# Optimization experiments

Hardware: AMD Instinct MI355X
Metric: run time of the kernel (lower is better)

Reference implementation:

```python
import jax, jax.numpy as jnp
import numpy as np

N_NODES = 100000
N_EDGES = 3200000
IN_DIM = 128
OUT_DIM = 128
BN_EPS = 1e-5
FILL_VALUE = 1.0  # improved_gcn=False -> self-loop weight 1.0 (2.0 if improved)


def setup_inputs() -> dict:
    key = jax.random.key(0)
    k1, k2, k3, k4 = jax.random.split(key, 4)
    node_features = jax.random.normal(k1, (N_NODES, IN_DIM), dtype=jnp.float32)
    edge_index = jax.random.randint(k2, (2, N_EDGES), 0, N_NODES, dtype=jnp.int64)
    edge_weight = jax.random.uniform(k3, (N_EDGES,), dtype=jnp.float32)
    # Glorot init like PyG GCNConv
    W = jax.random.normal(k4, (IN_DIM, OUT_DIM), dtype=jnp.float32) * np.sqrt(2.0 / (IN_DIM + OUT_DIM))
    b = jnp.zeros((OUT_DIM,), dtype=jnp.float32)
    gamma = jnp.ones((OUT_DIM,), dtype=jnp.float32)
    beta = jnp.zeros((OUT_DIM,), dtype=jnp.float32)
    return {"node_features": node_features, "edge_index": edge_index,
            "edge_weight": edge_weight, "W": W, "b": b, "gamma": gamma, "beta": beta}


def reference(node_features, edge_index, edge_weight, W, b, gamma, beta):
    N = node_features.shape[0]
    dt = node_features.dtype
    # --- gcn_norm: add self loops, symmetric normalization ---
    loop = jnp.arange(N, dtype=edge_index.dtype)
    row = jnp.concatenate([edge_index[0], loop])  # source
    col = jnp.concatenate([edge_index[1], loop])  # target (aggregation dim)
    w = jnp.concatenate([edge_weight.astype(dt), jnp.full((N,), FILL_VALUE, dtype=dt)])
    deg = jax.ops.segment_sum(w, col, num_segments=N)
    dinv = jnp.where(deg > 0, jax.lax.rsqrt(deg), 0.0).astype(dt)
    norm = dinv[row] * w * dinv[col]  # [E+N]
    # --- linear transform then message passing (scatter-add into targets) ---
    x = node_features @ W  # [N, out_dim]
    msg = x[row] * norm[:, None]  # [E+N, out_dim] gather
    out = jax.ops.segment_sum(msg, col, num_segments=N) + b
    # --- relu ---
    h = jax.nn.relu(out)
    # --- BatchNorm1d (training-mode batch statistics, biased variance) ---
    mean = jnp.mean(h, axis=0)
    var = jnp.mean(jnp.square(h - mean), axis=0)
    h = (h - mean) * jax.lax.rsqrt(var + BN_EPS) * gamma + beta
    # dropout is identity in eval / deterministic reference
    return h
```

## Files before the change

### kernel.cpp

```cpp
#include <hip/hip_runtime.h>
#include <hip/hip_bf16.h>


#define BKT_BITS 7
#define BKT_SZ 128
#define MAX_BKT 1024
#define CHUNK 8192

typedef __attribute__((ext_vector_type(8))) short bf16x8;
typedef __attribute__((ext_vector_type(4))) float f32x4;

__device__ __forceinline__ unsigned bf16rn(float f) {
    unsigned x = __float_as_uint(f);
    return (x + 0x7fffu + ((x >> 16) & 1u)) >> 16;
}
__device__ __forceinline__ float bflo(unsigned u) { return __uint_as_float(u << 16); }
__device__ __forceinline__ float bfhi(unsigned u) { return __uint_as_float(u & 0xffff0000u); }

__global__ __launch_bounds__(256) void k_bhist2(const int* __restrict__ col,
        int* __restrict__ blkoff, const float* __restrict__ Wm,
        unsigned* __restrict__ WT, int E, int nb, int nbc) {
    __shared__ int h[MAX_BKT];
    for (int i = threadIdx.x; i < nb; i += 256) h[i] = 0;
    __syncthreads();
    int base = blockIdx.x * CHUNK, lim = min(base + CHUNK, E);
    for (int e = base + threadIdx.x; e < lim; e += 256)
        atomicAdd(&h[col[e] >> BKT_BITS], 1);
    __syncthreads();
    for (int i = threadIdx.x; i < nb; i += 256)
        blkoff[(size_t)i * nbc + blockIdx.x] = h[i];
    if (blockIdx.x == 0) {
        for (int i = threadIdx.x; i < 128 * 64; i += 256) {
            int j = i >> 6, w = i & 63;
            float a = Wm[(size_t)(2 * w) * 128 + j];
            float b = Wm[(size_t)(2 * w + 1) * 128 + j];
            WT[i] = bf16rn(a) | (bf16rn(b) << 16);
        }
    }
}

__global__ void k_bscan2a(int* __restrict__ blkoff, int* __restrict__ btot,
                          int nb, int nbc) {
    int b = blockIdx.x * 256 + threadIdx.x;
    if (b >= nb) return;
    int* p = blkoff + (size_t)b * nbc;
    int run = 0;
#pragma unroll 4
    for (int i = 0; i < nbc; ++i) { int c = p[i]; p[i] = run; run += c; }
    btot[b] = run;
}

__global__ __launch_bounds__(1024) void k_bscan2b(const int* __restrict__ btot,
        int* __restrict__ bbase, int* __restrict__ ptr, float* __restrict__ sums,
        int nb, int N, int E) {
    __shared__ int ls[1024];
    int t = threadIdx.x;
    int v = (t < nb) ? btot[t] : 0;
    ls[t] = v;
    __syncthreads();
    for (int off = 1; off < 1024; off <<= 1) {
        int u = (t >= off) ? ls[t - off] : 0;
        __syncthreads();
        ls[t] += u;
        __syncthreads();
    }
    if (t < nb) bbase[t] = ls[t] - v;
    if (t == nb - 1) bbase[nb] = ls[t];
    if (t == 0) ptr[N] = E;
    if (t < 512) sums[t] = 0.0f;
}

__global__ __launch_bounds__(256) void k_passA3(
        const int* __restrict__ row, const int* __restrict__ col,
        const float* __restrict__ w, const int* __restrict__ blkoff,
        const int* __restrict__ bbase, unsigned* __restrict__ tmp,
        int E, int nb, int nbc) {
    __shared__ int cur[MAX_BKT];
    for (int i = threadIdx.x; i < nb; i += 256)
        cur[i] = bbase[i] + blkoff[(size_t)i * nbc + blockIdx.x];
    __syncthreads();
    int base = blockIdx.x * CHUNK, lim = min(base + CHUNK, E);
    for (int e = base + threadIdx.x; e < lim; e += 256) {
        int c = col[e];
        int q8 = (int)(w[e] * 256.0f + 0.5f);
        if (q8 > 255) q8 = 255;
        unsigned rec = ((unsigned)row[e] << 15) | ((unsigned)(c & 127) << 8) | (unsigned)q8;
        int pos = atomicAdd(&cur[c >> BKT_BITS], 1);
        tmp[pos] = rec;
    }
}

__global__ __launch_bounds__(256) void k_passB2(
        const unsigned* __restrict__ tmp, const int* __restrict__ bbase,
        unsigned* __restrict__ packed, int* __restrict__ ptr,
        float* __restrict__ dinv, int N) {
    __shared__ int hcnt[BKT_SZ];
    __shared__ int wsumi[BKT_SZ];
    __shared__ int cur[BKT_SZ];
    __shared__ float dcl[BKT_SZ];
    int b = blockIdx.x;
    int t = threadIdx.x;
    if (t < BKT_SZ) { hcnt[t] = 0; wsumi[t] = 0; }
    __syncthreads();
    int beg = bbase[b], end = bbase[b + 1];
    for (int k = beg + t; k < end; k += 256) {
        unsigned p = tmp[k];
        int li = (p >> 8) & 127;
        atomicAdd(&hcnt[li], 1);
        atomicAdd(&wsumi[li], (int)(p & 255u));
    }
    __syncthreads();
    if (t < BKT_SZ) cur[t] = hcnt[t];
    __syncthreads();
    for (int off = 1; off < BKT_SZ; off <<= 1) {
        int v = (t < BKT_SZ && t >= off) ? cur[t - off] : 0;
        __syncthreads();
        if (t < BKT_SZ) cur[t] += v;
        __syncthreads();
    }
    if (t < BKT_SZ) {
        int p = beg + cur[t] - hcnt[t];
        cur[t] = p;
        float d = 1.0f + (float)wsumi[t] * (1.0f / 256.0f);
        float dc = rsqrtf(d);
        dcl[t] = dc;
        int n = (b << BKT_BITS) + t;
        if (n < N) { ptr[n] = p; dinv[n] = dc; }
    }
    __syncthreads();
    for (int k = beg + t; k < end; k += 256) {
        unsigned p = tmp[k];
        int li = (p >> 8) & 127;
        int pos = atomicAdd(&cur[li], 1);
        float fw = (float)(p & 255u) * (1.0f / 256.0f) * dcl[li];
        unsigned wb = bf16rn(fw) & 0x7FFFu;
        packed[pos] = ((p >> 15) << 15) | wb;
    }
}

__global__ void k_conv2(const float* __restrict__ nf, const float* __restrict__ dinv,
                        uint4* __restrict__ tab, int N) {
    size_t i = (size_t)blockIdx.x * 256 + threadIdx.x;
    if (i >= (size_t)N * 16) return;
    int n = (int)(i >> 4);
    float dv = dinv[n];
    const float4* src = (const float4*)nf + 2 * i;
    float4 a = src[0], b = src[1];
    uint4 r;
    r.x = bf16rn(a.x * dv) | (bf16rn(a.y * dv) << 16);
    r.y = bf16rn(a.z * dv) | (bf16rn(a.w * dv) << 16);
    r.z = bf16rn(b.x * dv) | (bf16rn(b.y * dv) << 16);
    r.w = bf16rn(b.z * dv) | (bf16rn(b.w * dv) << 16);
    tab[i] = r;
}

#define EDGE_FMA(aX, nX, tX)                                     \
    aX[0] += nX * bflo(tX.x); aX[1] += nX * bfhi(tX.x);          \
    aX[2] += nX * bflo(tX.y); aX[3] += nX * bfhi(tX.y);          \
    aX[4] += nX * bflo(tX.z); aX[5] += nX * bfhi(tX.z);          \
    aX[6] += nX * bflo(tX.w); aX[7] += nX * bfhi(tX.w);

__global__ __launch_bounds__(256) void k_gatherq(
        const unsigned* __restrict__ packed, const int* __restrict__ ptr,
        const float* __restrict__ dinv, const unsigned* __restrict__ tab,
        unsigned* __restrict__ aggb, int N) {
    int lane = threadIdx.x & 63;
    int q = lane >> 4, fl = lane & 15;
    int wid = (int)(((size_t)blockIdx.x * 256 + threadIdx.x) >> 6);
    int node = wid * 4 + q;
    if (node >= N) return;
    int beg = ptr[node], end = ptr[node + 1];
    float dc = dinv[node];
    float a0[8] = {}, a1[8] = {}, a2[8] = {}, a3[8] = {};
    int k = beg;
    for (; k + 4 <= end; k += 4) {
        unsigned p0 = packed[k];
        unsigned p1 = packed[k + 1];
        unsigned p2 = packed[k + 2];
        unsigned p3 = packed[k + 3];
        uint4 t0 = *(const uint4*)(tab + (size_t)(p0 >> 15) * 64 + fl * 4);
        uint4 t1 = *(const uint4*)(tab + (size_t)(p1 >> 15) * 64 + fl * 4);
        uint4 t2 = *(const uint4*)(tab + (size_t)(p2 >> 15) * 64 + fl * 4);
        uint4 t3 = *(const uint4*)(tab + (size_t)(p3 >> 15) * 64 + fl * 4);
        float n0 = bflo(p0 & 0x7FFFu);
        float n1 = bflo(p1 & 0x7FFFu);
        float n2 = bflo(p2 & 0x7FFFu);
        float n3 = bflo(p3 & 0x7FFFu);
        EDGE_FMA(a0, n0, t0)
        EDGE_FMA(a1, n1, t1)
        EDGE_FMA(a2, n2, t2)
        EDGE_FMA(a3, n3, t3)
    }
    for (; k < end; ++k) {
        unsigned p = packed[k];
        uint4 t = *(const uint4*)(tab + (size_t)(p >> 15) * 64 + fl * 4);
        float n = bflo(p & 0x7FFFu);
        EDGE_FMA(a0, n, t)
    }
    {
        uint4 t = *(const uint4*)(tab + (size_t)node * 64 + fl * 4);
        EDGE_FMA(a0, dc, t)
    }
#pragma unroll
    for (int j = 0; j < 8; ++j) a0[j] = (a0[j] + a1[j]) + (a2[j] + a3[j]);
    uint4 r;
    r.x = bf16rn(a0[0]) | (bf16rn(a0[1]) << 16);
    r.y = bf16rn(a0[2]) | (bf16rn(a0[3]) << 16);
    r.z = bf16rn(a0[4]) | (bf16rn(a0[5]) << 16);
    r.w = bf16rn(a0[6]) | (bf16rn(a0[7]) << 16);
    *(uint4*)(aggb + (size_t)node * 64 + fl * 4) = r;
}

__global__ __launch_bounds__(256) void k_gatherwF(
        const unsigned* __restrict__ packed, const int* __restrict__ ptr,
        const float* __restrict__ dinv, const unsigned* __restrict__ tab,
        float* __restrict__ out, int N) {
    int wid = (int)(((size_t)blockIdx.x * 256 + threadIdx.x) >> 6);
    int lane = threadIdx.x & 63;
    if (wid >= N) return;
    int beg = ptr[wid], end = ptr[wid + 1];
    float dc = dinv[wid];
    int q = lane >> 4;
    int fl = lane & 15;
    float a0[8] = {}, a1[8] = {};
    int k = beg;
    for (; k + 8 <= end; k += 8) {
        unsigned p0 = packed[k + q];
        unsigned p1 = packed[k + 4 + q];
        uint4 t0 = *(const uint4*)(tab + (size_t)(p0 >> 15) * 64 + fl * 4);
        uint4 t1 = *(const uint4*)(tab + (size_t)(p1 >> 15) * 64 + fl * 4);
        float n0 = bflo(p0 & 0x7FFFu);
        float n1 = bflo(p1 & 0x7FFFu);
        EDGE_FMA(a0, n0, t0)
        EDGE_FMA(a1, n1, t1)
    }
    for (; k < end; k += 4) {
        int i0 = k + q;
        if (i0 < end) {
            unsigned p0 = packed[i0];
            uint4 t0 = *(const uint4*)(tab + (size_t)(p0 >> 15) * 64 + fl * 4);
            float n0 = bflo(p0 & 0x7FFFu);
            EDGE_FMA(a0, n0, t0)
        }
    }
#pragma unroll
    for (int j = 0; j < 8; ++j) {
        float s = a0[j] + a1[j];
        s += __shfl_xor(s, 16);
        s += __shfl_xor(s, 32);
        a0[j] = s;
    }
    if (q == 0) {
        uint4 t = *(const uint4*)(tab + (size_t)wid * 64 + fl * 4);
        EDGE_FMA(a0, dc, t)
        float4* dst = (float4*)(out + (size_t)wid * 128 + fl * 8);
        dst[0] = make_float4(a0[0], a0[1], a0[2], a0[3]);
        dst[1] = make_float4(a0[4], a0[5], a0[6], a0[7]);
    }
}

__global__ __launch_bounds__(256) void k_gemm3b(
        unsigned* aggb, const unsigned* __restrict__ WT,
        const float* __restrict__ bias, float* __restrict__ sums, int N) {
    __shared__ unsigned A_l[128][68];
    __shared__ unsigned W_l[128][68];
    __shared__ float bs[256];
    int tid = threadIdx.x;
    int r0 = blockIdx.x * 128;
    bs[tid] = 0.0f;
    {
        int j = tid >> 1, h = tid & 1;
        const uint4* src = (const uint4*)(WT + j * 64 + h * 32);
#pragma unroll
        for (int i = 0; i < 8; ++i)
            *(uint4*)&W_l[j][h * 32 + i * 4] = src[i];
    }
    {
        int j = tid >> 1, h = tid & 1;
        int gr = r0 + j;
        if (gr < N) {
            const uint4* src = (const uint4*)(aggb + (size_t)gr * 64 + h * 32);
#pragma unroll
            for (int i = 0; i < 8; ++i)
                *(uint4*)&A_l[j][h * 32 + i * 4] = src[i];
        } else {
            uint4 z = {0, 0, 0, 0};
#pragma unroll
            for (int i = 0; i < 8; ++i)
                *(uint4*)&A_l[j][h * 32 + i * 4] = z;
        }
    }
    __syncthreads();

    int wv = tid >> 6, l = tid & 63;
    int lr = l & 15, lk = l >> 4;
    f32x4 acc[2][8] = {};
#pragma unroll
    for (int ks = 0; ks < 4; ++ks) {
        bf16x8 a0 = *(bf16x8*)&A_l[wv * 32 + lr][ks * 16 + lk * 4];
        bf16x8 a1 = *(bf16x8*)&A_l[wv * 32 + 16 + lr][ks * 16 + lk * 4];
#pragma unroll
        for (int nt = 0; nt < 8; ++nt) {
            bf16x8 b = *(bf16x8*)&W_l[nt * 16 + lr][ks * 16 + lk * 4];
            acc[0][nt] = __builtin_amdgcn_mfma_f32_16x16x32_bf16(a0, b, acc[0][nt], 0, 0, 0);
            acc[1][nt] = __builtin_amdgcn_mfma_f32_16x16x32_bf16(a1, b, acc[1][nt], 0, 0, 0);
        }
    }

    unsigned short* ab = (unsigned short*)aggb;
#pragma unroll
    for (int nt = 0; nt < 8; ++nt) {
        int colc = nt * 16 + lr;
        float bc = bias[colc];
        float s = 0.0f, sq = 0.0f;
#pragma unroll
        for (int ms = 0; ms < 2; ++ms) {
#pragma unroll
            for (int p = 0; p < 4; ++p) {
                int rrow = r0 + wv * 32 + ms * 16 + lk * 4 + p;
                float v = fmaxf(acc[ms][nt][p] + bc, 0.0f);
                if (rrow < N) {
                    ab[(size_t)rrow * 128 + colc] = (unsigned short)bf16rn(v);
                    s += v;
                    sq += v * v;
                }
            }
        }
        s += __shfl_xor(s, 16);  s += __shfl_xor(s, 32);
        sq += __shfl_xor(sq, 16); sq += __shfl_xor(sq, 32);
        if (l < 16) {
            atomicAdd(&bs[colc], s);
            atomicAdd(&bs[128 + colc], sq);
        }
    }
    __syncthreads();
    if (tid < 128) {
        atomicAdd(&sums[tid], bs[tid]);
        atomicAdd(&sums[128 + tid], bs[128 + tid]);
    }
}

__global__ __launch_bounds__(256) void k_bnapplyB2(
        const unsigned* __restrict__ aggb, const float* __restrict__ sums,
        const float* __restrict__ gamma, const float* __restrict__ beta,
        float* __restrict__ out, size_t n16, int N) {
    __shared__ float sc[128], sh[128];
    int t = threadIdx.x;
    if (t < 128) {
        float inv_n = 1.0f / (float)N;
        float mean = sums[t] * inv_n;
        float var = sums[128 + t] * inv_n - mean * mean;
        float s = rsqrtf(var + 1e-5f) * gamma[t];
        sc[t] = s;
        sh[t] = beta[t] - mean * s;
    }
    __syncthreads();
    size_t i = (size_t)blockIdx.x * 256 + threadIdx.x;
    if (i >= n16) return;
    int g = (int)(i & 15);
    uint4 v = ((const uint4*)aggb)[i];
    float4 sc0 = *(float4*)&sc[g * 8];
    float4 sc1 = *(float4*)&sc[g * 8 + 4];
    float4 sh0 = *(float4*)&sh[g * 8];
    float4 sh1 = *(float4*)&sh[g * 8 + 4];
    float4 o0, o1;
    o0.x = bflo(v.x) * sc0.x + sh0.x;
    o0.y = bfhi(v.x) * sc0.y + sh0.y;
    o0.z = bflo(v.y) * sc0.z + sh0.z;
    o0.w = bfhi(v.y) * sc0.w + sh0.w;
    o1.x = bflo(v.z) * sc1.x + sh1.x;
    o1.y = bfhi(v.z) * sc1.y + sh1.y;
    o1.z = bflo(v.w) * sc1.z + sh1.z;
    o1.w = bfhi(v.w) * sc1.w + sh1.w;
    ((float4*)out)[2 * i] = o0;
    ((float4*)out)[2 * i + 1] = o1;
}

__global__ void k_bnfin(float* __restrict__ sums, const float* __restrict__ gamma,
                        const float* __restrict__ beta, int N) {
    int j = threadIdx.x;
    float inv_n = 1.0f / (float)N;
    float mean = sums[j] * inv_n;
    float var = sums[128 + j] * inv_n - mean * mean;
    float sc = rsqrtf(var + 1e-5f) * gamma[j];
    sums[256 + j] = sc;
    sums[384 + j] = beta[j] - mean * sc;
}

__global__ void k_bnapply(float* __restrict__ h, const float* __restrict__ sums, size_t n4) {
    size_t i = (size_t)blockIdx.x * 256 + threadIdx.x;
    if (i >= n4) return;
    int j4 = (int)(i & 31);
    float4 v = ((float4*)h)[i];
    float4 sc = ((const float4*)(sums + 256))[j4];
    float4 sh = ((const float4*)(sums + 384))[j4];
    v.x = v.x * sc.x + sh.x;
    v.y = v.y * sc.y + sh.y;
    v.z = v.z * sc.z + sh.z;
    v.w = v.w * sc.w + sh.w;
    ((float4*)h)[i] = v;
}

__global__ void k_init0(int* __restrict__ bcnt, float* __restrict__ sums, int nb) {
    int i = blockIdx.x * 256 + threadIdx.x;
    if (i < nb) bcnt[i] = 0;
    if (blockIdx.x == 0 && threadIdx.x < 512) sums[threadIdx.x] = 0.0f;
}
__global__ __launch_bounds__(256) void k_bhist(const int* __restrict__ col,
                                               int* __restrict__ bcnt, int E, int nb) {
    __shared__ int h[MAX_BKT];
    for (int i = threadIdx.x; i < nb; i += 256) h[i] = 0;
    __syncthreads();
    int base = blockIdx.x * CHUNK, lim = min(base + CHUNK, E);
    for (int e = base + threadIdx.x; e < lim; e += 256)
        atomicAdd(&h[col[e] >> BKT_BITS], 1);
    __syncthreads();
    for (int i = threadIdx.x; i < nb; i += 256) {
        int c = h[i];
        if (c) atomicAdd(&bcnt[i], c);
    }
}
__global__ __launch_bounds__(1024) void k_bscan(const int* __restrict__ bcnt,
        int* __restrict__ bbase, int* __restrict__ bcur,
        int* __restrict__ ptr, int nb, int N, int E) {
    __shared__ int ls[1024];
    int t = threadIdx.x;
    int v = (t < nb) ? bcnt[t] : 0;
    ls[t] = v;
    __syncthreads();
    for (int off = 1; off < 1024; off <<= 1) {
        int u = (t >= off) ? ls[t - off] : 0;
        __syncthreads();
        ls[t] += u;
        __syncthreads();
    }
    if (t < nb) {
        int ex = ls[t] - v;
        bbase[t] = ex;
        bcur[t] = ex;
    }
    if (t == nb - 1) bbase[nb] = ls[t];
    if (t == 0) ptr[N] = E;
}
__global__ __launch_bounds__(256) void k_passA2(
        const int* __restrict__ row, const int* __restrict__ col,
        const float* __restrict__ w, int* __restrict__ bcur,
        unsigned* __restrict__ tmp, int E, int nb) {
    __shared__ int h[MAX_BKT];
    for (int i = threadIdx.x; i < nb; i += 256) h[i] = 0;
    __syncthreads();
    int base = blockIdx.x * CHUNK, lim = min(base + CHUNK, E);
    for (int e = base + threadIdx.x; e < lim; e += 256)
        atomicAdd(&h[col[e] >> BKT_BITS], 1);
    __syncthreads();
    for (int i = threadIdx.x; i < nb; i += 256) {
        int c = h[i];
        if (c) h[i] = atomicAdd(&bcur[i], c);
    }
    __syncthreads();
    for (int e = base + threadIdx.x; e < lim; e += 256) {
        int c = col[e];
        int q8 = (int)(w[e] * 256.0f + 0.5f);
        if (q8 > 255) q8 = 255;
        unsigned rec = ((unsigned)row[e] << 15) | ((unsigned)(c & 127) << 8) | (unsigned)q8;
        int pos = atomicAdd(&h[c >> BKT_BITS], 1);
        tmp[pos] = rec;
    }
}

__global__ void k_init(int* __restrict__ cnt, float* __restrict__ sums, int N) {
    int i = blockIdx.x * 256 + threadIdx.x;
    if (i < N) cnt[i] = 0;
    if (blockIdx.x == 0 && threadIdx.x < 512) sums[threadIdx.x] = 0.0f;
}
__global__ void k_count(const int* __restrict__ col, int* __restrict__ cnt, int E) {
    int e = blockIdx.x * 256 + threadIdx.x;
    if (e < E) atomicAdd(&cnt[col[e]], 1);
}
__global__ __launch_bounds__(256) void kS1(const int* __restrict__ cnt,
                                           int* __restrict__ ptr,
                                           int* __restrict__ bsum, int N) {
    __shared__ int ls[256];
    int t = threadIdx.x, i = blockIdx.x * 256 + t;
    int v = (i < N) ? cnt[i] : 0;
    ls[t] = v;
    __syncthreads();
    for (int off = 1; off < 256; off <<= 1) {
        int u = (t >= off) ? ls[t - off] : 0;
        __syncthreads();
        ls[t] += u;
        __syncthreads();
    }
    if (i < N) ptr[i] = ls[t] - v;
    if (t == 255) bsum[blockIdx.x] = ls[255];
}
__global__ __launch_bounds__(512) void kS2(int* __restrict__ bsum,
                                           int* __restrict__ ptr, int NB, int N) {
    __shared__ int ls[512];
    int t = threadIdx.x;
    int chunk = (NB + 511) / 512;
    int b = t * chunk, e = min(b + chunk, NB);
    int s = 0;
    for (int i = b; i < e; ++i) s += bsum[i];
    ls[t] = s;
    __syncthreads();
    for (int off = 1; off < 512; off <<= 1) {
        int u = (t >= off) ? ls[t - off] : 0;
        __syncthreads();
        ls[t] += u;
        __syncthreads();
    }
    int run = ls[t] - s;
    for (int i = b; i < e; ++i) { int c = bsum[i]; bsum[i] = run; run += c; }
    if (t == 511) ptr[N] = ls[511];
}
__global__ void kS3(int* __restrict__ ptr, int* __restrict__ cnt,
                    const int* __restrict__ bsum, int N) {
    int i = blockIdx.x * 256 + threadIdx.x;
    if (i >= N) return;
    int p = ptr[i] + bsum[blockIdx.x];
    ptr[i] = p;
    cnt[i] = p;
}
__global__ void k_fill(const int* __restrict__ row, const int* __restrict__ col,
                       const float* __restrict__ w, int* __restrict__ cursor,
                       int2* __restrict__ packed, int E) {
    int e = blockIdx.x * 256 + threadIdx.x;
    if (e < E) {
        int pos = atomicAdd(&cursor[col[e]], 1);
        packed[pos] = make_int2(row[e], __float_as_int(w[e]));
    }
}
__global__ __launch_bounds__(256) void k_degw(const int2* __restrict__ packed,
                                              const int* __restrict__ ptr,
                                              float* __restrict__ dinv, int N) {
    int wid = (int)(((size_t)blockIdx.x * 256 + threadIdx.x) >> 6);
    int lane = threadIdx.x & 63;
    if (wid >= N) return;
    int beg = ptr[wid], end = ptr[wid + 1];
    float s = 0.0f;
    for (int k = beg + lane; k < end; k += 64) s += __int_as_float(packed[k].y);
#pragma unroll
    for (int off = 32; off; off >>= 1) s += __shfl_xor(s, off);
    if (lane == 0) {
        float d = 1.0f + s;
        dinv[wid] = d > 0.0f ? rsqrtf(d) : 0.0f;
    }
}
__global__ __launch_bounds__(256) void k_gather(
        const int2* __restrict__ packed, const int* __restrict__ ptr,
        const float* __restrict__ dinv, const float* __restrict__ nf,
        float* __restrict__ out, int N) {
    int wid = (int)(((size_t)blockIdx.x * 256 + threadIdx.x) >> 6);
    int lane = threadIdx.x & 63;
    if (wid >= N) return;
    int c = wid;
    int beg = ptr[c], end = ptr[c + 1];
    float dc = dinv[c];
    int half = lane >> 5;
    int fl = lane & 31;
    float4 acc = {0.f, 0.f, 0.f, 0.f};
    for (int k = beg; k < end; k += 2) {
        int idx = k + half;
        bool v = idx < end;
        int2 p = packed[v ? idx : beg];
        float nrm = v ? dc * __int_as_float(p.y) * dinv[p.x] : 0.0f;
        float4 x = ((const float4*)(nf + (size_t)p.x * 128))[fl];
        acc.x += nrm * x.x; acc.y += nrm * x.y;
        acc.z += nrm * x.z; acc.w += nrm * x.w;
    }
    acc.x += __shfl_xor(acc.x, 32);
    acc.y += __shfl_xor(acc.y, 32);
    acc.z += __shfl_xor(acc.z, 32);
    acc.w += __shfl_xor(acc.w, 32);
    if (half == 0) {
        float s2 = dc * dc;
        float4 sf = ((const float4*)(nf + (size_t)c * 128))[fl];
        acc.x += s2 * sf.x; acc.y += s2 * sf.y;
        acc.z += s2 * sf.z; acc.w += s2 * sf.w;
        ((float4*)(out + (size_t)c * 128))[fl] = acc;
    }
}
__global__ void k_initA(float* __restrict__ deg, float* __restrict__ sums, int N) {
    int i = blockIdx.x * 256 + threadIdx.x;
    if (i < N) deg[i] = 1.0f;
    if (blockIdx.x == 0 && threadIdx.x < 512) sums[threadIdx.x] = 0.0f;
}
__global__ void k_deg(const int* __restrict__ col, const float* __restrict__ w,
                      float* __restrict__ deg, int E) {
    int e = blockIdx.x * 256 + threadIdx.x;
    if (e < E) atomicAdd(&deg[col[e]], w[e]);
}
__global__ void k_dinv(float* __restrict__ deg, int N) {
    int i = blockIdx.x * 256 + threadIdx.x;
    if (i < N) { float d = deg[i]; deg[i] = d > 0.0f ? rsqrtf(d) : 0.0f; }
}
__global__ void k_self(const float* __restrict__ nf, const float* __restrict__ dinv,
                       float* __restrict__ agg, int N) {
    size_t i = (size_t)blockIdx.x * 256 + threadIdx.x;
    if (i >= (size_t)N * 32) return;
    int node = (int)(i >> 5);
    float s = dinv[node]; s = s * s;
    float4 v = ((const float4*)nf)[i];
    v.x *= s; v.y *= s; v.z *= s; v.w *= s;
    ((float4*)agg)[i] = v;
}
__global__ __launch_bounds__(256) void k_scatter(
        const int* __restrict__ row, const int* __restrict__ col,
        const float* __restrict__ w, const float* __restrict__ dinv,
        const float* __restrict__ nf, float* __restrict__ agg, int E) {
    int wid = (int)(((size_t)blockIdx.x * blockDim.x + threadIdx.x) >> 6);
    int lane = threadIdx.x & 63;
    if (wid >= E) return;
    int r = row[wid], c = col[wid];
    float nrm = dinv[r] * w[wid] * dinv[c];
    float2 v = ((const float2*)(nf + (size_t)r * 128))[lane];
    float* dst = agg + (size_t)c * 128 + lane * 2;
    atomicAdd(dst, v.x * nrm);
    atomicAdd(dst + 1, v.y * nrm);
}

__global__ __launch_bounds__(256) void k_gemm2(float* __restrict__ h,
        const float* __restrict__ W, const float* __restrict__ bias,
        float* __restrict__ sums, int N) {
    __shared__ float At[2][32][132];
    __shared__ float Wt[2][32][132];
    int tid = threadIdx.x;
    int tx = tid & 15, ty = tid >> 4;
    int r0 = blockIdx.x * 128;
#define STAGE_A(buf, k0)                                                     \
    _Pragma("unroll")                                                        \
    for (int i = 0; i < 4; ++i) {                                            \
        int idx = tid + 256 * i;                                             \
        int row = idx >> 3, c4 = idx & 7;                                    \
        int gr = r0 + row; if (gr > N - 1) gr = N - 1;                       \
        float4 v = *(const float4*)&h[(size_t)gr * 128 + (k0) + c4 * 4];     \
        At[buf][c4 * 4 + 0][row] = v.x;                                      \
        At[buf][c4 * 4 + 1][row] = v.y;                                      \
        At[buf][c4 * 4 + 2][row] = v.z;                                      \
        At[buf][c4 * 4 + 3][row] = v.w;                                      \
    }
#define STAGE_W(buf, k0)                                                     \
    _Pragma("unroll")                                                        \
    for (int i = 0; i < 4; ++i) {                                            \
        int idx = tid + 256 * i;                                             \
        int kk = idx >> 5, c4 = idx & 31;                                    \
        float4 v = *(const float4*)&W[(size_t)((k0) + kk) * 128 + c4 * 4];   \
        *(float4*)&Wt[buf][kk][c4 * 4] = v;                                  \
    }
    STAGE_A(0, 0)
    STAGE_W(0, 0)
    float acc[8][8] = {};
    for (int t = 0; t < 4; ++t) {
        __syncthreads();
        if (t < 3) {
            int nb = (t + 1) & 1;
            STAGE_A(nb, (t + 1) * 32)
            STAGE_W(nb, (t + 1) * 32)
        }
        int kb = t & 1;
#pragma unroll
        for (int k = 0; k < 32; ++k) {
            float a[8], w[8];
            *(float4*)&a[0] = *(float4*)&At[kb][k][ty * 8];
            *(float4*)&a[4] = *(float4*)&At[kb][k][ty * 8 + 4];
            *(float4*)&w[0] = *(float4*)&Wt[kb][k][tx * 8];
            *(float4*)&w[4] = *(float4*)&Wt[kb][k][tx * 8 + 4];
#pragma unroll
            for (int r = 0; r < 8; ++r)
#pragma unroll
                for (int cc = 0; cc < 8; ++cc)
                    acc[r][cc] += a[r] * w[cc];
        }
    }
    float bv[8];
    *(float4*)&bv[0] = *(const float4*)&bias[tx * 8];
    *(float4*)&bv[4] = *(const float4*)&bias[tx * 8 + 4];
    float s[8] = {}, sq[8] = {};
#pragma unroll
    for (int r = 0; r < 8; ++r) {
        int gr = r0 + ty * 8 + r;
        if (gr < N) {
            float o[8];
#pragma unroll
            for (int cc = 0; cc < 8; ++cc) {
                o[cc] = fmaxf(acc[r][cc] + bv[cc], 0.0f);
                s[cc] += o[cc];
                sq[cc] += o[cc] * o[cc];
            }
            float4* dst = (float4*)&h[(size_t)gr * 128 + tx * 8];
            dst[0] = make_float4(o[0], o[1], o[2], o[3]);
            dst[1] = make_float4(o[4], o[5], o[6], o[7]);
        }
    }
    float* ls = &At[0][0][0];
    __syncthreads();
#pragma unroll
    for (int cc = 0; cc < 8; ++cc) {
        ls[ty * 128 + tx * 8 + cc] = s[cc];
        ls[2048 + ty * 128 + tx * 8 + cc] = sq[cc];
    }
    __syncthreads();
    if (tid < 128) {
        float ssum = 0.f, sqsum = 0.f;
#pragma unroll
        for (int u = 0; u < 16; ++u) {
            ssum += ls[u * 128 + tid];
            sqsum += ls[2048 + u * 128 + tid];
        }
        atomicAdd(&sums[tid], ssum);
        atomicAdd(&sums[128 + tid], sqsum);
    }
#undef STAGE_A
#undef STAGE_W
}

extern "C" void kernel_launch(void* const* d_in, const int* in_sizes, int n_in,
                              void* d_out, int out_size, void* d_ws, size_t ws_size,
                              hipStream_t stream) {
    const float* nf    = (const float*)d_in[0];
    const int*   ei    = (const int*)d_in[1];
    const float* ew    = (const float*)d_in[2];
    const float* W     = (const float*)d_in[3];
    const float* bias  = (const float*)d_in[4];
    const float* gamma = (const float*)d_in[5];
    const float* beta  = (const float*)d_in[6];
    float* out = (float*)d_out;

    const int N = in_sizes[0] / 128;
    const int E = in_sizes[2];
    const int* row = ei;
    const int* col = ei + E;

    int nb_n  = (N + 255) / 256;
    int nb_e  = (E + 255) / 256;
    int nb_w  = (int)(((size_t)N + 3) / 4);
    int nb_q  = (N + 15) / 16;
    int nb_v4 = (int)(((size_t)N * 32 + 255) / 256);
    int nbk   = (N + BKT_SZ - 1) >> BKT_BITS;
    int nb_c  = (E + CHUNK - 1) / CHUNK;
    int nconv = (int)(((size_t)N * 16 + 255) / 256);
    size_t n16 = (size_t)N * 16;
    size_t tt_words = (size_t)64 * N > (size_t)E ? (size_t)64 * N : (size_t)E;

    float* dinv = (float*)d_ws;
    int*   ptr  = (int*)d_ws + N;
    float* sums = (float*)d_ws + 2 * N + 1;
    int*   bbase1 = (int*)d_ws + 2 * N + 513;
    int*   btot   = bbase1 + nbk + 1;
    int*   blkoff = btot + nbk;
    size_t wt_off = ((size_t)(2 * N + 514 + 2 * nbk) + (size_t)nbk * nb_c + 3) & ~(size_t)3;
    unsigned* wtb = (unsigned*)((int*)d_ws + wt_off);
    size_t pk_off = (wt_off + 8192 + 3) & ~(size_t)3;
    unsigned* p1_packed = (unsigned*)((int*)d_ws + pk_off);
    size_t tt_off = (pk_off + (size_t)E + 3) & ~(size_t)3;
    unsigned* p1_tmp = (unsigned*)((int*)d_ws + tt_off);
    unsigned* p1_tab = (unsigned*)((int*)d_ws + tt_off);
    size_t ab_off = (tt_off + tt_words + 3) & ~(size_t)3;
    unsigned* aggb = (unsigned*)((int*)d_ws + ab_off);
    size_t need_p1 = (ab_off + (size_t)64 * N) * 4;

    float* dinv2 = (float*)d_ws;
    int*   ptr2  = (int*)d_ws + N;
    int*   cnt3  = (int*)d_ws + 2 * N + 1;
    float* sums2 = (float*)d_ws + 3 * N + 1;
    int*   bsum2 = (int*)d_ws + 3 * N + 513;
    int*   bbase2 = (int*)d_ws + 3 * N + 1025;
    int*   bcur2  = bbase2 + nbk + 1;
    size_t pk2 = ((size_t)(3 * N + 1026 + 2 * nbk) + 3) & ~(size_t)3;
    unsigned* packed2 = (unsigned*)((int*)d_ws + pk2);
    size_t tt2 = (pk2 + (size_t)E + 3) & ~(size_t)3;
    unsigned* tmp2 = (unsigned*)((int*)d_ws + tt2);
    unsigned* tab2 = (unsigned*)((int*)d_ws + tt2);
    size_t need_full2 = (tt2 + tt_words) * 4;

    int2*  packed3 = (int2*)((int*)d_ws + pk2);
    size_t need_csr3 = (pk2 + (size_t)2 * E) * 4;

    if (nbk <= MAX_BKT && ws_size >= need_p1) {
        k_bhist2<<<nb_c, 256, 0, stream>>>(col, blkoff, W, wtb, E, nbk, nb_c);
        k_bscan2a<<<(nbk + 255) / 256, 256, 0, stream>>>(blkoff, btot, nbk, nb_c);
        k_bscan2b<<<1, 1024, 0, stream>>>(btot, bbase1, ptr, sums, nbk, N, E);
        k_passA3<<<nb_c, 256, 0, stream>>>(row, col, ew, blkoff, bbase1, p1_tmp, E, nbk, nb_c);
        k_passB2<<<nbk, 256, 0, stream>>>(p1_tmp, bbase1, p1_packed, ptr, dinv, N);
        k_conv2<<<nconv, 256, 0, stream>>>(nf, dinv, (uint4*)p1_tab, N);
        k_gatherq<<<nb_q, 256, 0, stream>>>(p1_packed, ptr, dinv, p1_tab, aggb, N);
        k_gemm3b<<<(N + 127) / 128, 256, 0, stream>>>(aggb, wtb, bias, sums, N);
        k_bnapplyB2<<<(int)((n16 + 255) / 256), 256, 0, stream>>>(aggb, sums, gamma, beta, out, n16, N);
        return;
    }

    if (nbk <= MAX_BKT && ws_size >= need_full2) {
        k_init0<<<(max(nbk, 512) + 255) / 256, 256, 0, stream>>>(bcur2, sums2, nbk);
        k_bhist<<<nb_c, 256, 0, stream>>>(col, bcur2, E, nbk);
        k_bscan<<<1, 1024, 0, stream>>>(bcur2, bbase2, bcur2, ptr2, nbk, N, E);
        k_passA2<<<nb_c, 256, 0, stream>>>(row, col, ew, bcur2, tmp2, E, nbk);
        k_passB2<<<nbk, 256, 0, stream>>>(tmp2, bbase2, packed2, ptr2, dinv2, N);
        k_conv2<<<nconv, 256, 0, stream>>>(nf, dinv2, (uint4*)tab2, N);
        k_gatherwF<<<nb_w, 256, 0, stream>>>(packed2, ptr2, dinv2, tab2, out, N);
        k_gemm2<<<(N + 127) / 128, 256, 0, stream>>>(out, W, bias, sums2, N);
        k_bnfin<<<1, 128, 0, stream>>>(sums2, gamma, beta, N);
        k_bnapply<<<nb_v4, 256, 0, stream>>>(out, sums2, (size_t)N * 32);
        return;
    }

    if (ws_size >= need_csr3) {
        k_init<<<nb_n, 256, 0, stream>>>(cnt3, sums2, N);
        k_count<<<nb_e, 256, 0, stream>>>(col, cnt3, E);
        kS1<<<nb_n, 256, 0, stream>>>(cnt3, ptr2, bsum2, N);
        kS2<<<1, 512, 0, stream>>>(bsum2, ptr2, nb_n, N);
        kS3<<<nb_n, 256, 0, stream>>>(ptr2, cnt3, bsum2, N);
        k_fill<<<nb_e, 256, 0, stream>>>(row, col, ew, cnt3, packed3, E);
        k_degw<<<nb_w, 256, 0, stream>>>(packed3, ptr2, dinv2, N);
        k_gather<<<nb_w, 256, 0, stream>>>(packed3, ptr2, dinv2, nf, out, N);
        k_gemm2<<<(N + 127) / 128, 256, 0, stream>>>(out, W, bias, sums2, N);
        k_bnfin<<<1, 128, 0, stream>>>(sums2, gamma, beta, N);
        k_bnapply<<<nb_v4, 256, 0, stream>>>(out, sums2, (size_t)N * 32);
        return;
    }

    {
        float* deg = (float*)d_ws;
        float* sm  = (float*)d_ws + N;
        k_initA<<<nb_n, 256, 0, stream>>>(deg, sm, N);
        k_deg<<<nb_e, 256, 0, stream>>>(col, ew, deg, E);
        k_dinv<<<nb_n, 256, 0, stream>>>(deg, N);
        k_self<<<nb_v4, 256, 0, stream>>>(nf, deg, out, N);
        k_scatter<<<(E + 3) / 4, 256, 0, stream>>>(row, col, ew, deg, nf, out, E);
        k_gemm2<<<(N + 127) / 128, 256, 0, stream>>>(out, W, bias, sm, N);
        k_bnfin<<<1, 128, 0, stream>>>(sm, gamma, beta, N);
        k_bnapply<<<nb_v4, 256, 0, stream>>>(out, sm, (size_t)N * 32);
    }
}
```

Baseline: 337.3 us.

## Use one wave per node in gather, merge scans, read W directly in GEMM

```diff
diff --git a/kernel.cpp b/kernel.cpp
--- a/kernel.cpp
+++ b/kernel.cpp
@@ -39,24 +39,17 @@
     }
 }
 
-__global__ void k_bscan2a(int* __restrict__ blkoff, int* __restrict__ btot,
-                          int nb, int nbc) {
-    int b = blockIdx.x * 256 + threadIdx.x;
-    if (b >= nb) return;
-    int* p = blkoff + (size_t)b * nbc;
-    int run = 0;
-#pragma unroll 4
-    for (int i = 0; i < nbc; ++i) { int c = p[i]; p[i] = run; run += c; }
-    btot[b] = run;
-}
-
-__global__ __launch_bounds__(1024) void k_bscan2b(const int* __restrict__ btot,
+__global__ __launch_bounds__(1024) void k_bscanM(int* __restrict__ blkoff,
         int* __restrict__ bbase, int* __restrict__ ptr, float* __restrict__ sums,
-        int nb, int N, int E) {
+        int nb, int nbc, int N, int E) {
     __shared__ int ls[1024];
     int t = threadIdx.x;
-    int v = (t < nb) ? btot[t] : 0;
-    ls[t] = v;
+    int run = 0;
+    if (t < nb) {
+        int* p = blkoff + (size_t)t * nbc;
+        for (int i = 0; i < nbc; ++i) { int c = p[i]; p[i] = run; run += c; }
+    }
+    ls[t] = run;
     __syncthreads();
     for (int off = 1; off < 1024; off <<= 1) {
         int u = (t >= off) ? ls[t - off] : 0;
@@ -64,7 +57,7 @@
         ls[t] += u;
         __syncthreads();
     }
-    if (t < nb) bbase[t] = ls[t] - v;
+    if (t < nb) bbase[t] = ls[t] - run;
     if (t == nb - 1) bbase[nb] = ls[t];
     if (t == 0) ptr[N] = E;
     if (t < 512) sums[t] = 0.0f;
@@ -160,24 +153,24 @@
     aX[4] += nX * bflo(tX.z); aX[5] += nX * bfhi(tX.z);          \
     aX[6] += nX * bflo(tX.w); aX[7] += nX * bfhi(tX.w);
 
-__global__ __launch_bounds__(256) void k_gatherq(
+__global__ __launch_bounds__(256) void k_gatherw5(
         const unsigned* __restrict__ packed, const int* __restrict__ ptr,
         const float* __restrict__ dinv, const unsigned* __restrict__ tab,
         unsigned* __restrict__ aggb, int N) {
+    int wid = (int)(((size_t)blockIdx.x * 256 + threadIdx.x) >> 6);
     int lane = threadIdx.x & 63;
-    int q = lane >> 4, fl = lane & 15;
-    int wid = (int)(((size_t)blockIdx.x * 256 + threadIdx.x) >> 6);
-    int node = wid * 4 + q;
-    if (node >= N) return;
-    int beg = ptr[node], end = ptr[node + 1];
-    float dc = dinv[node];
+    if (wid >= N) return;
+    int beg = ptr[wid], end = ptr[wid + 1];
+    float dc = dinv[wid];
+    int q = lane >> 4;
+    int fl = lane & 15;
     float a0[8] = {}, a1[8] = {}, a2[8] = {}, a3[8] = {};
     int k = beg;
-    for (; k + 4 <= end; k += 4) {
-        unsigned p0 = packed[k];
-        unsigned p1 = packed[k + 1];
-        unsigned p2 = packed[k + 2];
-        unsigned p3 = packed[k + 3];
+    for (; k + 16 <= end; k += 16) {
+        unsigned p0 = packed[k + q];
+        unsigned p1 = packed[k + 4 + q];
+        unsigned p2 = packed[k + 8 + q];
+        unsigned p3 = packed[k + 12 + q];
         uint4 t0 = *(const uint4*)(tab + (size_t)(p0 >> 15) * 64 + fl * 4);
         uint4 t1 = *(const uint4*)(tab + (size_t)(p1 >> 15) * 64 + fl * 4);
         uint4 t2 = *(const uint4*)(tab + (size_t)(p2 >> 15) * 64 + fl * 4);
@@ -191,24 +184,43 @@
         EDGE_FMA(a2, n2, t2)
         EDGE_FMA(a3, n3, t3)
     }
-    for (; k < end; ++k) {
-        unsigned p = packed[k];
-        uint4 t = *(const uint4*)(tab + (size_t)(p >> 15) * 64 + fl * 4);
-        float n = bflo(p & 0x7FFFu);
-        EDGE_FMA(a0, n, t)
-    }
-    {
-        uint4 t = *(const uint4*)(tab + (size_t)node * 64 + fl * 4);
+    if (k + 8 <= end) {
+        unsigned p0 = packed[k + q];
+        unsigned p1 = packed[k + 4 + q];
+        uint4 t0 = *(const uint4*)(tab + (size_t)(p0 >> 15) * 64 + fl * 4);
+        uint4 t1 = *(const uint4*)(tab + (size_t)(p1 >> 15) * 64 + fl * 4);
+        float n0 = bflo(p0 & 0x7FFFu);
+        float n1 = bflo(p1 & 0x7FFFu);
+        EDGE_FMA(a0, n0, t0)
+        EDGE_FMA(a1, n1, t1)
+        k += 8;
+    }
+    for (; k < end; k += 4) {
+        int i0 = k + q;
+        if (i0 < end) {
+            unsigned p0 = packed[i0];
+            uint4 t0 = *(const uint4*)(tab + (size_t)(p0 >> 15) * 64 + fl * 4);
+            float n0 = bflo(p0 & 0x7FFFu);
+            EDGE_FMA(a0, n0, t0)
+        }
+    }
+#pragma unroll
+    for (int j = 0; j < 8; ++j) {
+        float s = (a0[j] + a1[j]) + (a2[j] + a3[j]);
+        s += __shfl_xor(s, 16);
+        s += __shfl_xor(s, 32);
+        a0[j] = s;
+    }
+    if (q == 0) {
+        uint4 t = *(const uint4*)(tab + (size_t)wid * 64 + fl * 4);
         EDGE_FMA(a0, dc, t)
-    }
-#pragma unroll
-    for (int j = 0; j < 8; ++j) a0[j] = (a0[j] + a1[j]) + (a2[j] + a3[j]);
-    uint4 r;
-    r.x = bf16rn(a0[0]) | (bf16rn(a0[1]) << 16);
-    r.y = bf16rn(a0[2]) | (bf16rn(a0[3]) << 16);
-    r.z = bf16rn(a0[4]) | (bf16rn(a0[5]) << 16);
-    r.w = bf16rn(a0[6]) | (bf16rn(a0[7]) << 16);
-    *(uint4*)(aggb + (size_t)node * 64 + fl * 4) = r;
+        uint4 r;
+        r.x = bf16rn(a0[0]) | (bf16rn(a0[1]) << 16);
+        r.y = bf16rn(a0[2]) | (bf16rn(a0[3]) << 16);
+        r.z = bf16rn(a0[4]) | (bf16rn(a0[5]) << 16);
+        r.w = bf16rn(a0[6]) | (bf16rn(a0[7]) << 16);
+        *(uint4*)(aggb + (size_t)wid * 64 + fl * 4) = r;
+    }
 }
 
 __global__ __launch_bounds__(256) void k_gatherwF(
@@ -259,24 +271,16 @@
     }
 }
 
-__global__ __launch_bounds__(256) void k_gemm3b(
+__global__ __launch_bounds__(256) void k_gemm4(
         unsigned* aggb, const unsigned* __restrict__ WT,
         const float* __restrict__ bias, float* __restrict__ sums, int N) {
     __shared__ unsigned A_l[128][68];
-    __shared__ unsigned W_l[128][68];
     __shared__ float bs[256];
     int tid = threadIdx.x;
     int r0 = blockIdx.x * 128;
     bs[tid] = 0.0f;
     {
         int j = tid >> 1, h = tid & 1;
-        const uint4* src = (const uint4*)(WT + j * 64 + h * 32);
-#pragma unroll
-        for (int i = 0; i < 8; ++i)
-            *(uint4*)&W_l[j][h * 32 + i * 4] = src[i];
-    }
-    {
-        int j = tid >> 1, h = tid & 1;
         int gr = r0 + j;
         if (gr < N) {
             const uint4* src = (const uint4*)(aggb + (size_t)gr * 64 + h * 32);
@@ -301,7 +305,7 @@
         bf16x8 a1 = *(bf16x8*)&A_l[wv * 32 + 16 + lr][ks * 16 + lk * 4];
 #pragma unroll
         for (int nt = 0; nt < 8; ++nt) {
-            bf16x8 b = *(bf16x8*)&W_l[nt * 16 + lr][ks * 16 + lk * 4];
+            bf16x8 b = *(const bf16x8*)(WT + (size_t)(nt * 16 + lr) * 64 + ks * 16 + lk * 4);
             acc[0][nt] = __builtin_amdgcn_mfma_f32_16x16x32_bf16(a0, b, acc[0][nt], 0, 0, 0);
             acc[1][nt] = __builtin_amdgcn_mfma_f32_16x16x32_bf16(a1, b, acc[1][nt], 0, 0, 0);
         }
@@ -735,7 +739,6 @@
     int nb_n  = (N + 255) / 256;
     int nb_e  = (E + 255) / 256;
     int nb_w  = (int)(((size_t)N + 3) / 4);
-    int nb_q  = (N + 15) / 16;
     int nb_v4 = (int)(((size_t)N * 32 + 255) / 256);
     int nbk   = (N + BKT_SZ - 1) >> BKT_BITS;
     int nb_c  = (E + CHUNK - 1) / CHUNK;
@@ -779,13 +782,12 @@
 
     if (nbk <= MAX_BKT && ws_size >= need_p1) {
         k_bhist2<<<nb_c, 256, 0, stream>>>(col, blkoff, W, wtb, E, nbk, nb_c);
-        k_bscan2a<<<(nbk + 255) / 256, 256, 0, stream>>>(blkoff, btot, nbk, nb_c);
-        k_bscan2b<<<1, 1024, 0, stream>>>(btot, bbase1, ptr, sums, nbk, N, E);
+        k_bscanM<<<1, 1024, 0, stream>>>(blkoff, bbase1, ptr, sums, nbk, nb_c, N, E);
         k_passA3<<<nb_c, 256, 0, stream>>>(row, col, ew, blkoff, bbase1, p1_tmp, E, nbk, nb_c);
         k_passB2<<<nbk, 256, 0, stream>>>(p1_tmp, bbase1, p1_packed, ptr, dinv, N);
         k_conv2<<<nconv, 256, 0, stream>>>(nf, dinv, (uint4*)p1_tab, N);
-        k_gatherq<<<nb_q, 256, 0, stream>>>(p1_packed, ptr, dinv, p1_tab, aggb, N);
-        k_gemm3b<<<(N + 127) / 128, 256, 0, stream>>>(aggb, wtb, bias, sums, N);
+        k_gatherw5<<<nb_w, 256, 0, stream>>>(p1_packed, ptr, dinv, p1_tab, aggb, N);
+        k_gemm4<<<(N + 127) / 128, 256, 0, stream>>>(aggb, wtb, bias, sums, N);
         k_bnapplyB2<<<(int)((n16 + 255) / 256), 256, 0, stream>>>(aggb, sums, gamma, beta, out, n16, N);
         return;
     }
```

Measured after the change: 851.9 us. 2.53x slower.
